# Kernel optimization log

Measured on AMD Instinct MI355X. Metric: run time of the kernel, lower is better.

The kernel has to match this reference:

```python
import jax, jax.numpy as jnp
import numpy as np

N = 50000      # nodes
E = 1_600_000  # edges (avg degree 32)
D = 128        # in/hidden channels
OUT = 64       # out channels


def setup_inputs() -> dict:
    key = jax.random.key(0)
    ks = jax.random.split(key, 12)
    s = 0.08  # ~glorot scale for 128-dim
    return {
        "x": jax.random.normal(ks[0], (N, D), jnp.float32),
        "edge_index": jax.random.randint(ks[1], (2, E), 0, N, dtype=jnp.int64),
        # GCN layer 1
        "W1": jax.random.normal(ks[2], (D, D), jnp.float32) * s,
        "b1": jnp.zeros((D,), jnp.float32),
        # GraphSAGE layer 2 (mean aggregation): lin_l on neighbors, lin_r on root
        "Wl": jax.random.normal(ks[3], (D, D), jnp.float32) * s,
        "Wr": jax.random.normal(ks[4], (D, D), jnp.float32) * s,
        "bs": jnp.zeros((D,), jnp.float32),
        # GAT layer 3 (heads=1, concat=False)
        "Wg": jax.random.normal(ks[5], (D, D), jnp.float32) * s,
        "a_s": jax.random.normal(ks[6], (D,), jnp.float32) * s,
        "a_d": jax.random.normal(ks[7], (D,), jnp.float32) * s,
        "bg": jnp.zeros((D,), jnp.float32),
        # GCN output layer
        "Wo": jax.random.normal(ks[8], (D, OUT), jnp.float32) * s,
        "bo": jnp.zeros((OUT,), jnp.float32),
    }


def _self_loops(src, dst, n):
    loop = jnp.arange(n, dtype=src.dtype)
    return jnp.concatenate([src, loop]), jnp.concatenate([dst, loop])


def gcn_conv(x, W, b, src, dst, n):
    # PyG GCNConv: add self-loops, symmetric normalization D^-1/2 (A+I) D^-1/2
    s2, d2 = _self_loops(src, dst, n)
    deg = jax.ops.segment_sum(jnp.ones_like(d2, dtype=x.dtype), d2, num_segments=n)
    dinv = jnp.where(deg > 0, jax.lax.rsqrt(deg), 0.0)
    h = x @ W                         # [n, out]
    norm = dinv[s2] * dinv[d2]        # [E+n]
    out = jax.ops.segment_sum(h[s2] * norm[:, None], d2, num_segments=n)
    return out + b


def sage_conv(x, Wl, Wr, b, src, dst, n):
    # PyG SAGEConv, aggr='mean': W_l * mean_neigh + W_r * x (no self-loops)
    deg = jax.ops.segment_sum(jnp.ones_like(dst, dtype=x.dtype), dst, num_segments=n)
    agg = jax.ops.segment_sum(x[src], dst, num_segments=n)
    mean = agg / jnp.maximum(deg, 1.0)[:, None]
    return mean @ Wl + x @ Wr + b


def gat_conv(x, W, a_s, a_d, b, src, dst, n):
    # PyG GATConv heads=1, concat=False: self-loops, edge softmax over incoming edges
    h = x @ W                               # [n, out]
    s2, d2 = _self_loops(src, dst, n)
    alpha_src = h @ a_s                     # [n]
    alpha_dst = h @ a_d                     # [n]
    e = jax.nn.leaky_relu(alpha_src[s2] + alpha_dst[d2], negative_slope=0.2)
    m = jax.ops.segment_max(e, d2, num_segments=n)   # every node has a self-loop
    ex = jnp.exp(e - m[d2])
    denom = jax.ops.segment_sum(ex, d2, num_segments=n)
    alpha = ex / denom[d2]
    out = jax.ops.segment_sum(alpha[:, None] * h[s2], d2, num_segments=n)
    return out + b


def reference(x, edge_index, W1, b1, Wl, Wr, bs, Wg, a_s, a_d, bg, Wo, bo):
    src, dst = edge_index[0], edge_index[1]
    n = x.shape[0]
    # eval mode: F.dropout(training=False) is identity
    h = jax.nn.relu(gcn_conv(x, W1, b1, src, dst, n))
    h = jax.nn.relu(sage_conv(h, Wl, Wr, bs, src, dst, n))
    h = jax.nn.relu(gat_conv(h, Wg, a_s, a_d, bg, src, dst, n))
    return gcn_conv(h, Wo, bo, src, dst, n)
```

## Files before the change

### kernel.cpp

```cpp
#include <hip/hip_runtime.h>
#include <math.h>


#define BUCKET_BITS 8
#define BUCKET_SZ   256
#define NBMAX       256
#define CAP         10240
#define CAPE        2048

typedef short short8 __attribute__((ext_vector_type(8)));
typedef float f32x4 __attribute__((ext_vector_type(4)));
typedef unsigned int u32x4 __attribute__((ext_vector_type(4)));
typedef unsigned short u16x8 __attribute__((ext_vector_type(8)));

__device__ __forceinline__ float leaky02(float x) { return x > 0.0f ? x : 0.2f * x; }
__device__ __forceinline__ float bflo(unsigned u) { return __uint_as_float(u << 16); }
__device__ __forceinline__ float bfhi(unsigned u) { return __uint_as_float(u & 0xFFFF0000u); }
__device__ __forceinline__ unsigned short f2bf(float f) {
    unsigned u = __float_as_uint(f);
    u += 0x7FFFu + ((u >> 16) & 1u);
    return (unsigned short)(u >> 16);
}

template<int NO, bool AFP32, bool SCALE, bool BIASRELU, bool DUAL, bool DOTS>
__global__ __launch_bounds__(256) void mgemm_k(
    const void* __restrict__ Av, const float* __restrict__ W,
    const void* __restrict__ A1v, const float* __restrict__ W1,
    unsigned short* __restrict__ C16,
    const float* __restrict__ scale, const float* __restrict__ bias,
    const float* __restrict__ a_s, const float* __restrict__ a_d,
    float* __restrict__ as_, float* __restrict__ ad_, int n)
{
    constexpr int CT = NO / 16;
    __shared__ unsigned short Wp[128 * NO];
    const int tid = threadIdx.x;
    const int wave = tid >> 6, lane = tid & 63;
    const int q = lane >> 4, ml = lane & 15;
    const int row0 = blockIdx.x * 64 + wave * 16;
    int arow = row0 + ml; if (arow >= n) arow = n - 1;

    f32x4 acc[CT];
#pragma unroll
    for (int c = 0; c < CT; c++) acc[c] = {0.f, 0.f, 0.f, 0.f};

    for (int half = 0; half < (DUAL ? 2 : 1); half++) {
        const float* Wsrc = half ? W1 : W;
        const void* Asrc = half ? A1v : Av;
        __syncthreads();
        for (int f = tid; f < 64 * (NO / 4); f += 256) {
            const int kp = f / (NO / 4);
            const int n4 = f % (NO / 4);
            const float4 a = *(const float4*)(Wsrc + (size_t)(2 * kp) * NO + n4 * 4);
            const float4 b = *(const float4*)(Wsrc + (size_t)(2 * kp + 1) * NO + n4 * 4);
            const int k = 2 * kp, kb = k >> 5, qq = (k >> 3) & 3, p = (k & 7) >> 1;
            const float av[4] = {a.x, a.y, a.z, a.w};
            const float bv[4] = {b.x, b.y, b.z, b.w};
#pragma unroll
            for (int j = 0; j < 4; j++) {
                int col = n4 * 4 + j;
                int c = col >> 4, nl = col & 15;
                unsigned pk = (unsigned)f2bf(av[j]) | ((unsigned)f2bf(bv[j]) << 16);
                ((unsigned*)Wp)[(((kb * CT + c) * 64) + qq * 16 + nl) * 4 + p] = pk;
            }
        }
        __syncthreads();
#pragma unroll
        for (int kb = 0; kb < 4; kb++) {
            short8 afr;
            if (AFP32) {
                const float* Af = (const float*)Asrc + (size_t)arow * 128 + kb * 32 + q * 8;
#pragma unroll
                for (int j = 0; j < 8; j++) afr[j] = (short)f2bf(Af[j]);
            } else {
                afr = *(const short8*)((const unsigned short*)Asrc +
                                       (size_t)arow * 128 + kb * 32 + q * 8);
            }
#pragma unroll
            for (int c = 0; c < CT; c++) {
                short8 bfr = *(const short8*)(Wp + ((size_t)(kb * CT + c) * 64 + lane) * 8);
                acc[c] = __builtin_amdgcn_mfma_f32_16x16x32_bf16(afr, bfr, acc[c], 0, 0, 0);
            }
        }
    }

    if (DOTS) {
        float ps[4] = {0.f, 0.f, 0.f, 0.f}, pd[4] = {0.f, 0.f, 0.f, 0.f};
#pragma unroll
        for (int c = 0; c < CT; c++) {
            float sv = a_s[c * 16 + ml], dv = a_d[c * 16 + ml];
#pragma unroll
            for (int r = 0; r < 4; r++) {
                ps[r] = fmaf(acc[c][r], sv, ps[r]);
                pd[r] = fmaf(acc[c][r], dv, pd[r]);
            }
        }
#pragma unroll
        for (int off = 1; off < 16; off <<= 1) {
#pragma unroll
            for (int r = 0; r < 4; r++) {
                ps[r] += __shfl_xor(ps[r], off, 64);
                pd[r] += __shfl_xor(pd[r], off, 64);
            }
        }
        if (ml == 0) {
#pragma unroll
            for (int r = 0; r < 4; r++) {
                int row = row0 + q * 4 + r;
                if (row < n) { as_[row] = ps[r]; ad_[row] = pd[r]; }
            }
        }
    }

    float sc[4];
    if (SCALE) {
#pragma unroll
        for (int r = 0; r < 4; r++) {
            int row = row0 + q * 4 + r;
            sc[r] = scale[row < n ? row : 0];
        }
    }
#pragma unroll
    for (int c = 0; c < CT; c++) {
        float bv = BIASRELU ? bias[c * 16 + ml] : 0.0f;
#pragma unroll
        for (int r = 0; r < 4; r++) {
            int row = row0 + q * 4 + r;
            if (row < n) {
                float v = acc[c][r];
                if (SCALE) v *= sc[r];
                if (BIASRELU) v = fmaxf(v + bv, 0.0f);
                C16[(size_t)row * NO + c * 16 + ml] = f2bf(v);
            }
        }
    }
}

__global__ void binit_k(int* __restrict__ bcur, int nb) {
    int t = threadIdx.x;
    if (t < nb) bcur[t] = t * CAP;
}

#define PART_CH 4096
__global__ __launch_bounds__(256) void part_k(
    const int* __restrict__ src, const int* __restrict__ dst,
    int* __restrict__ bcur, unsigned long long* __restrict__ part, int nE)
{
    __shared__ int cnt[NBMAX];
    __shared__ int cur[NBMAX];
    const int base = blockIdx.x * PART_CH;
    const int t = threadIdx.x;
    cnt[t] = 0;
    __syncthreads();
    int d[PART_CH / 256], s[PART_CH / 256];
#pragma unroll
    for (int j = 0; j < PART_CH / 256; j++) {
        int e = base + j * 256 + t;
        if (e < nE) {
            d[j] = dst[e]; s[j] = src[e];
            atomicAdd(&cnt[d[j] >> BUCKET_BITS], 1);
        } else d[j] = -1;
    }
    __syncthreads();
    {
        int c = cnt[t];
        cur[t] = c ? atomicAdd(&bcur[t], c) : 0;
    }
    __syncthreads();
#pragma unroll
    for (int j = 0; j < PART_CH / 256; j++) {
        if (d[j] >= 0) {
            int p = atomicAdd(&cur[d[j] >> BUCKET_BITS], 1);
            part[p] = ((unsigned long long)(unsigned)d[j] << 32) | (unsigned)s[j];
        }
    }
}

__global__ __launch_bounds__(256) void bscan_k(const int* __restrict__ bcur,
                                               int* __restrict__ bofs, int nb) {
    __shared__ int sm[256];
    const int t = threadIdx.x;
    int v = (t < nb) ? (bcur[t] - t * CAP) : 0;
    sm[t] = v;
    __syncthreads();
    for (int off = 1; off < 256; off <<= 1) {
        int tv = (t >= off) ? sm[t - off] : 0;
        __syncthreads();
        sm[t] += tv;
        __syncthreads();
    }
    if (t < nb) {
        bofs[t] = sm[t] - v;
        if (t == nb - 1) bofs[nb] = sm[t];
    }
}

__global__ __launch_bounds__(256) void csr_k(
    const unsigned long long* __restrict__ part, const int* __restrict__ bcur,
    const int* __restrict__ bofs, int* __restrict__ rowptr, int* __restrict__ srcs,
    float* __restrict__ dinv, float* __restrict__ invm, int n, int nE)
{
    __shared__ int lcnt[BUCKET_SZ];
    __shared__ int sm[BUCKET_SZ];
    __shared__ int lcur[BUCKET_SZ];
    const int b = blockIdx.x;
    const int t = threadIdx.x;
    const int base_in = b * CAP;
    const int cntE = bcur[b] - base_in;
    const int base_out = bofs[b];

    lcnt[t] = 0;
    __syncthreads();
#pragma unroll 4
    for (int e = t; e < cntE; e += 256) {
        int dl = (int)(part[base_in + e] >> 32) & (BUCKET_SZ - 1);
        atomicAdd(&lcnt[dl], 1);
    }
    __syncthreads();
    int v = lcnt[t];
    sm[t] = v;
    __syncthreads();
    for (int off = 1; off < 256; off <<= 1) {
        int tv = (t >= off) ? sm[t - off] : 0;
        __syncthreads();
        sm[t] += tv;
        __syncthreads();
    }
    const int excl = sm[t] - v;
    const int node = (b << BUCKET_BITS) + t;
    if (node < n) {
        rowptr[node] = base_out + excl;
        float dg = (float)v;
        dinv[node] = rsqrtf(dg + 1.0f);
        invm[node] = 1.0f / fmaxf(dg, 1.0f);
        if (node == n - 1) rowptr[n] = nE;
    }
    lcur[t] = excl;
    __syncthreads();
#pragma unroll 4
    for (int e = t; e < cntE; e += 256) {
        unsigned long long w = part[base_in + e];
        int dl = (int)(w >> 32) & (BUCKET_SZ - 1);
        int pos = atomicAdd(&lcur[dl], 1);
        srcs[base_out + pos] = (int)(unsigned)w;
    }
}

template<int LPN, int MODE, bool OV>
__device__ __forceinline__ void gath_loop(
    const u32x4* __restrict__ H4, const int* __restrict__ srcs,
    const int* lsrc, const float* lw, const float* __restrict__ as_,
    float ad_d, int beg, int end, int beg_blk, int lane, float* acc)
{
    const u32x4* __restrict__ Hl = H4 + lane;
    int k = beg;
    for (; k + 8 <= end; k += 8) {
        unsigned sidx[8]; float wv[8];
#pragma unroll
        for (int j = 0; j < 8; j++) {
            int ofs = k + j - beg_blk;
            if (OV) {
                int ofc = ofs < CAPE ? ofs : CAPE - 1;
                int s = (ofs < CAPE) ? lsrc[ofc] : srcs[k + j];
                sidx[j] = (unsigned)s;
                if (MODE == 2)
                    wv[j] = (ofs < CAPE) ? lw[ofc] : __expf(leaky02(as_[s] + ad_d));
            } else {
                sidx[j] = (unsigned)lsrc[ofs];
                if (MODE == 2) wv[j] = lw[ofs];
            }
        }
        u32x4 h[8];
#pragma unroll
        for (int j = 0; j < 8; j++) h[j] = Hl[(size_t)sidx[j] * LPN];
#pragma unroll
        for (int j = 0; j < 8; j++) {
#pragma unroll
            for (int c = 0; c < 4; c++) {
                if (MODE == 2) {
                    acc[2 * c]     = fmaf(wv[j], bflo(h[j][c]), acc[2 * c]);
                    acc[2 * c + 1] = fmaf(wv[j], bfhi(h[j][c]), acc[2 * c + 1]);
                } else {
                    acc[2 * c]     += bflo(h[j][c]);
                    acc[2 * c + 1] += bfhi(h[j][c]);
                }
            }
        }
    }
    if (k < end) {
        unsigned sidx[8]; float wv[8];
#pragma unroll
        for (int j = 0; j < 8; j++) {
            int kk = k + j;
            bool act = kk < end;
            int kc = act ? kk : end - 1;
            int ofs = kc - beg_blk;
            int s; float w0 = 1.0f;
            if (OV) {
                int ofc = ofs < CAPE ? ofs : CAPE - 1;
                s = (ofs < CAPE) ? lsrc[ofc] : srcs[kc];
                if (MODE == 2)
                    w0 = (ofs < CAPE) ? lw[ofc] : __expf(leaky02(as_[s] + ad_d));
            } else {
                s = lsrc[ofs];
                if (MODE == 2) w0 = lw[ofs];
            }
            sidx[j] = (unsigned)s;
            wv[j] = act ? w0 : 0.0f;
        }
        u32x4 h[8];
#pragma unroll
        for (int j = 0; j < 8; j++) h[j] = Hl[(size_t)sidx[j] * LPN];
#pragma unroll
        for (int j = 0; j < 8; j++) {
#pragma unroll
            for (int c = 0; c < 4; c++) {
                acc[2 * c]     = fmaf(wv[j], bflo(h[j][c]), acc[2 * c]);
                acc[2 * c + 1] = fmaf(wv[j], bfhi(h[j][c]), acc[2 * c + 1]);
            }
        }
    }
}

template<int F, int MODE>
__global__ __launch_bounds__(256) void gatherbf_k(
    const unsigned short* __restrict__ H16, float* __restrict__ outf,
    unsigned short* __restrict__ out16,
    const int* __restrict__ rowptr, const int* __restrict__ srcs,
    const float* __restrict__ dinv, const float* __restrict__ as_,
    const float* __restrict__ ad_, const float* __restrict__ bias, int n)
{
    constexpr int LPN = F / 8;
    constexpr int NPB = 256 / LPN;
    __shared__ int lsrc[CAPE];
    __shared__ float lw[(MODE == 2) ? CAPE : 1];

    const int tid = (int)threadIdx.x;
    const int node0 = (int)blockIdx.x * NPB;
    const int nodeN = min(node0 + NPB, n);
    const int beg_blk = rowptr[node0];
    const int end_blk = rowptr[nodeN];
    const int cnt = end_blk - beg_blk;
    const int cl = min(cnt, CAPE);
    for (int i = tid; i < cl; i += 256) lsrc[i] = srcs[beg_blk + i];
    __syncthreads();

    const int node = node0 + tid / LPN;
    const int lane = tid & (LPN - 1);
    const bool alive = node < n;
    int beg = 0, end = 0;
    if (alive) { beg = rowptr[node]; end = rowptr[node + 1]; }

    float ad_d = 0.f, rden = 0.f, sw = 0.f;
    if (MODE == 2) {
        if (alive) {
            ad_d = ad_[node];
            float self_e = __expf(leaky02(as_[node] + ad_d));
            float psum = 0.f;
            for (int kk = beg + lane; kk < end; kk += LPN) {
                int ofs = kk - beg_blk;
                int s = (ofs < CAPE) ? lsrc[ofs < CAPE ? ofs : 0] : srcs[kk];
                float wv = __expf(leaky02(as_[s] + ad_d));
                if (ofs < CAPE) lw[ofs] = wv;
                psum += wv;
            }
#pragma unroll
            for (int off = LPN / 2; off > 0; off >>= 1)
                psum += __shfl_xor(psum, off, 64);
            rden = 1.0f / (psum + self_e);
            sw = self_e * rden;
        }
        __syncthreads();
    }

    float acc[8];
#pragma unroll
    for (int j = 0; j < 8; j++) acc[j] = 0.f;

    const u32x4* __restrict__ H4 = (const u32x4*)H16;
    if (alive) {
        if (cnt <= CAPE)
            gath_loop<LPN, MODE, false>(H4, srcs, lsrc, lw, as_, ad_d,
                                        beg, end, beg_blk, lane, acc);
        else
            gath_loop<LPN, MODE, true>(H4, srcs, lsrc, lw, as_, ad_d,
                                       beg, end, beg_blk, lane, acc);
    }
    if (!alive) return;

    const size_t orow = (size_t)node * LPN + lane;
    float r[8];
    if (MODE == 0) {
        float sc = dinv[node];
#pragma unroll
        for (int j = 0; j < 8; j++) r[j] = acc[j] * sc;
    } else {
        u32x4 su = H4[orow];
        float sv[8];
#pragma unroll
        for (int c = 0; c < 4; c++) { sv[2 * c] = bflo(su[c]); sv[2 * c + 1] = bfhi(su[c]); }
        const float4* b4 = (const float4*)bias;
        float4 ba = b4[lane * 2], bb = b4[lane * 2 + 1];
        float bv[8] = {ba.x, ba.y, ba.z, ba.w, bb.x, bb.y, bb.z, bb.w};
        if (MODE == 2) {
#pragma unroll
            for (int j = 0; j < 8; j++)
                r[j] = fmaxf(fmaf(rden, acc[j], fmaf(sw, sv[j], bv[j])), 0.f);
        } else {
            float dv = dinv[node];
#pragma unroll
            for (int j = 0; j < 8; j++) {
                r[j] = dv * (acc[j] + sv[j]) + bv[j];
                if (MODE == 1) r[j] = fmaxf(r[j], 0.f);
            }
        }
    }
    if (MODE == 3) {
        float4 ra = {r[0], r[1], r[2], r[3]}, rb = {r[4], r[5], r[6], r[7]};
        ((float4*)outf)[orow * 2]     = ra;
        ((float4*)outf)[orow * 2 + 1] = rb;
    } else {
        u16x8 qv;
#pragma unroll
        for (int j = 0; j < 8; j++) qv[j] = f2bf(r[j]);
        ((u16x8*)out16)[orow] = qv;
    }
}

extern "C" void kernel_launch(void* const* d_in, const int* in_sizes, int n_in,
                              void* d_out, int out_size, void* d_ws, size_t ws_size,
                              hipStream_t stream)
{
    const float* x   = (const float*)d_in[0];
    const int*   ei  = (const int*)d_in[1];
    const float* W1  = (const float*)d_in[2];
    const float* b1  = (const float*)d_in[3];
    const float* Wl  = (const float*)d_in[4];
    const float* Wr  = (const float*)d_in[5];
    const float* bs  = (const float*)d_in[6];
    const float* Wg  = (const float*)d_in[7];
    const float* a_s = (const float*)d_in[8];
    const float* a_d = (const float*)d_in[9];
    const float* bg  = (const float*)d_in[10];
    const float* Wo  = (const float*)d_in[11];
    const float* bo  = (const float*)d_in[12];

    const int n  = in_sizes[0] / 128;
    const int nE = in_sizes[1] / 2;
    const int* src = ei;
    const int* dst = ei + nE;

    char* w = (char*)d_ws;
    auto alloc = [&](size_t bytes) { char* p = w; w += (bytes + 255) & ~(size_t)255; return p; };
    unsigned short* S0 = (unsigned short*)alloc((size_t)n * 128 * 2);
    unsigned short* S1 = (unsigned short*)alloc((size_t)n * 128 * 2);
    unsigned short* S2 = (unsigned short*)alloc((size_t)n * 128 * 2);
    const int nbv = (n + BUCKET_SZ - 1) / BUCKET_SZ;
    unsigned long long* part = (unsigned long long*)alloc((size_t)nbv * CAP * 8);
    int*   srcs   = (int*)alloc((size_t)nE * 4);
    int*   rowptr = (int*)alloc((size_t)(n + 1) * 4);
    int*   bofs   = (int*)alloc((NBMAX + 1) * 4);
    int*   bcur   = (int*)alloc(NBMAX * 4);
    float* dinv   = (float*)alloc((size_t)n * 4);
    float* invm   = (float*)alloc((size_t)n * 4);
    float* as_    = (float*)alloc((size_t)n * 4);
    float* ad_    = (float*)alloc((size_t)n * 4);

    const int TB = 256;
    auto cdiv = [](long long a, long long b) { return (int)((a + b - 1) / b); };
    const int nb     = nbv;
    const int gPart  = cdiv(nE, PART_CH);
    const int gGemm  = cdiv(n, 64);
    const int gGa128 = cdiv(n, 16);
    const int gGa64  = cdiv(n, 32);

    binit_k<<<1, 256, 0, stream>>>(bcur, nb);
    part_k<<<gPart, TB, 0, stream>>>(src, dst, bcur, part, nE);
    bscan_k<<<1, 256, 0, stream>>>(bcur, bofs, nb);
    csr_k<<<nb, TB, 0, stream>>>(part, bcur, bofs, rowptr, srcs, dinv, invm, n, nE);

    mgemm_k<128, true, true, false, false, false><<<gGemm, TB, 0, stream>>>(
        x, W1, nullptr, nullptr, S0, dinv, nullptr, nullptr, nullptr, nullptr, nullptr, n);
    gatherbf_k<128, 1><<<gGa128, TB, 0, stream>>>(S0, nullptr, S1, rowptr, srcs,
                                                  dinv, nullptr, nullptr, b1, n);

    gatherbf_k<128, 0><<<gGa128, TB, 0, stream>>>(S1, nullptr, S0, rowptr, srcs,
                                                  invm, nullptr, nullptr, nullptr, n);
    mgemm_k<128, false, false, true, true, false><<<gGemm, TB, 0, stream>>>(
        S0, Wl, S1, Wr, S2, nullptr, bs, nullptr, nullptr, nullptr, nullptr, n);

    mgemm_k<128, false, false, false, false, true><<<gGemm, TB, 0, stream>>>(
        S2, Wg, nullptr, nullptr, S1, nullptr, nullptr, a_s, a_d, as_, ad_, n);
    gatherbf_k<128, 2><<<gGa128, TB, 0, stream>>>(S1, nullptr, S0, rowptr, srcs,
                                                  nullptr, as_, ad_, bg, n);

    mgemm_k<64, false, true, false, false, false><<<gGemm, TB, 0, stream>>>(
        S0, Wo, nullptr, nullptr, S2, dinv, nullptr, nullptr, nullptr, nullptr, nullptr, n);
    gatherbf_k<64, 3><<<gGa64, TB, 0, stream>>>(S2, (float*)d_out, nullptr, rowptr, srcs,
                                                dinv, nullptr, nullptr, bo, n);
}
```

Baseline: 369.8 us.

## Store bf16 features in column-block-major layout and split gathers by column block

Feature matrices move from row-major to a column-blocked layout of 32 bf16 columns per block. Each gather block now handles 64 nodes for one 32-column slice, with blocks interleaved so that every slice shares the same node groups. The goal is a per-pass working set small enough to stay in L2/MALL, cutting the cost of random gathers. GAT edge weights and softmax denominators move into a separate gatw_k kernel that writes them to global memory, and CAPE is raised. The cost is an extra kernel, an extra edge-weight array to write and read, and srcs/rowptr being reread once per column block.

```diff
diff --git a/kernel.cpp b/kernel.cpp
--- a/kernel.cpp
+++ b/kernel.cpp
@@ -6,7 +6,7 @@
 #define BUCKET_SZ   256
 #define NBMAX       256
 #define CAP         10240
-#define CAPE        2048
+#define CAPE        2560
 
 typedef short short8 __attribute__((ext_vector_type(8)));
 typedef float f32x4 __attribute__((ext_vector_type(4)));
@@ -73,7 +73,7 @@
                 for (int j = 0; j < 8; j++) afr[j] = (short)f2bf(Af[j]);
             } else {
                 afr = *(const short8*)((const unsigned short*)Asrc +
-                                       (size_t)arow * 128 + kb * 32 + q * 8);
+                                       ((size_t)kb * n + arow) * 32 + q * 8);
             }
 #pragma unroll
             for (int c = 0; c < CT; c++) {
@@ -122,6 +122,7 @@
 #pragma unroll
     for (int c = 0; c < CT; c++) {
         float bv = BIASRELU ? bias[c * 16 + ml] : 0.0f;
+        const int col = c * 16 + ml;
 #pragma unroll
         for (int r = 0; r < 4; r++) {
             int row = row0 + q * 4 + r;
@@ -129,7 +130,7 @@
                 float v = acc[c][r];
                 if (SCALE) v *= sc[r];
                 if (BIASRELU) v = fmaxf(v + bv, 0.0f);
-                C16[(size_t)row * NO + c * 16 + ml] = f2bf(v);
+                C16[((size_t)(col >> 5) * n + row) * 32 + (col & 31)] = f2bf(v);
             }
         }
     }
@@ -245,13 +246,38 @@
     }
 }
 
-template<int LPN, int MODE, bool OV>
+__global__ __launch_bounds__(256) void gatw_k(
+    const int* __restrict__ rowptr, const int* __restrict__ srcs,
+    const float* __restrict__ as_, const float* __restrict__ ad_,
+    float* __restrict__ ew, float* __restrict__ rdn_, float* __restrict__ sw_, int n)
+{
+    const int node = blockIdx.x * 32 + (threadIdx.x >> 3);
+    const int lane = threadIdx.x & 7;
+    if (node >= n) return;
+    const int beg = rowptr[node], end = rowptr[node + 1];
+    const float ad_d = ad_[node];
+    float psum = 0.f;
+    for (int k = beg + lane; k < end; k += 8) {
+        float e = __expf(leaky02(as_[srcs[k]] + ad_d));
+        ew[k] = e;
+        psum += e;
+    }
+#pragma unroll
+    for (int off = 4; off > 0; off >>= 1) psum += __shfl_xor(psum, off, 64);
+    if (lane == 0) {
+        float se = __expf(leaky02(as_[node] + ad_d));
+        float r = 1.0f / (psum + se);
+        rdn_[node] = r;
+        sw_[node] = se * r;
+    }
+}
+
+template<int MODE, bool OV>
 __device__ __forceinline__ void gath_loop(
-    const u32x4* __restrict__ H4, const int* __restrict__ srcs,
-    const int* lsrc, const float* lw, const float* __restrict__ as_,
-    float ad_d, int beg, int end, int beg_blk, int lane, float* acc)
-{
-    const u32x4* __restrict__ Hl = H4 + lane;
+    const u32x4* __restrict__ Hc, const int* __restrict__ srcs,
+    const float* __restrict__ ew, const int* lsrc, const float* lw,
+    int beg, int end, int beg_blk, int lane, float* acc)
+{
     int k = beg;
     for (; k + 8 <= end; k += 8) {
         unsigned sidx[8]; float wv[8];
@@ -259,11 +285,10 @@
         for (int j = 0; j < 8; j++) {
             int ofs = k + j - beg_blk;
             if (OV) {
-                int ofc = ofs < CAPE ? ofs : CAPE - 1;
-                int s = (ofs < CAPE) ? lsrc[ofc] : srcs[k + j];
-                sidx[j] = (unsigned)s;
-                if (MODE == 2)
-                    wv[j] = (ofs < CAPE) ? lw[ofc] : __expf(leaky02(as_[s] + ad_d));
+                bool in = ofs < CAPE;
+                int ofc = in ? ofs : 0;
+                sidx[j] = (unsigned)(in ? lsrc[ofc] : srcs[k + j]);
+                if (MODE == 2) wv[j] = in ? lw[ofc] : ew[k + j];
             } else {
                 sidx[j] = (unsigned)lsrc[ofs];
                 if (MODE == 2) wv[j] = lw[ofs];
@@ -271,7 +296,7 @@
         }
         u32x4 h[8];
 #pragma unroll
-        for (int j = 0; j < 8; j++) h[j] = Hl[(size_t)sidx[j] * LPN];
+        for (int j = 0; j < 8; j++) h[j] = Hc[(size_t)sidx[j] * 4 + lane];
 #pragma unroll
         for (int j = 0; j < 8; j++) {
 #pragma unroll
@@ -296,10 +321,10 @@
             int ofs = kc - beg_blk;
             int s; float w0 = 1.0f;
             if (OV) {
-                int ofc = ofs < CAPE ? ofs : CAPE - 1;
-                s = (ofs < CAPE) ? lsrc[ofc] : srcs[kc];
-                if (MODE == 2)
-                    w0 = (ofs < CAPE) ? lw[ofc] : __expf(leaky02(as_[s] + ad_d));
+                bool in = ofs < CAPE;
+                int ofc = in ? ofs : 0;
+                s = in ? lsrc[ofc] : srcs[kc];
+                if (MODE == 2) w0 = in ? lw[ofc] : ew[kc];
             } else {
                 s = lsrc[ofs];
                 if (MODE == 2) w0 = lw[ofs];
@@ -309,7 +334,7 @@
         }
         u32x4 h[8];
 #pragma unroll
-        for (int j = 0; j < 8; j++) h[j] = Hl[(size_t)sidx[j] * LPN];
+        for (int j = 0; j < 8; j++) h[j] = Hc[(size_t)sidx[j] * 4 + lane];
 #pragma unroll
         for (int j = 0; j < 8; j++) {
 #pragma unroll
@@ -321,92 +346,77 @@
     }
 }
 
-template<int F, int MODE>
+template<int NCB, int MODE>
 __global__ __launch_bounds__(256) void gatherbf_k(
     const unsigned short* __restrict__ H16, float* __restrict__ outf,
     unsigned short* __restrict__ out16,
     const int* __restrict__ rowptr, const int* __restrict__ srcs,
-    const float* __restrict__ dinv, const float* __restrict__ as_,
-    const float* __restrict__ ad_, const float* __restrict__ bias, int n)
-{
-    constexpr int LPN = F / 8;
-    constexpr int NPB = 256 / LPN;
+    const float* __restrict__ scl,
+    const float* __restrict__ sw_,
+    const float* __restrict__ ew,
+    const float* __restrict__ bias, int n)
+{
+    constexpr int XPC = 8 / NCB;
+    constexpr int NPB = 64;
     __shared__ int lsrc[CAPE];
     __shared__ float lw[(MODE == 2) ? CAPE : 1];
 
+    const int bid = (int)blockIdx.x;
+    const int xj = bid & 7;
+    const int cb = xj / XPC;
+    const int NG = (n + NPB - 1) / NPB;
+    const int ng = (bid >> 3) * XPC + (xj % XPC);
+    if (ng >= NG) return;
+
     const int tid = (int)threadIdx.x;
-    const int node0 = (int)blockIdx.x * NPB;
+    const int node0 = ng * NPB;
     const int nodeN = min(node0 + NPB, n);
     const int beg_blk = rowptr[node0];
     const int end_blk = rowptr[nodeN];
     const int cnt = end_blk - beg_blk;
     const int cl = min(cnt, CAPE);
-    for (int i = tid; i < cl; i += 256) lsrc[i] = srcs[beg_blk + i];
-    __syncthreads();
-
-    const int node = node0 + tid / LPN;
-    const int lane = tid & (LPN - 1);
-    const bool alive = node < n;
-    int beg = 0, end = 0;
-    if (alive) { beg = rowptr[node]; end = rowptr[node + 1]; }
-
-    float ad_d = 0.f, rden = 0.f, sw = 0.f;
-    if (MODE == 2) {
-        if (alive) {
-            ad_d = ad_[node];
-            float self_e = __expf(leaky02(as_[node] + ad_d));
-            float psum = 0.f;
-            for (int kk = beg + lane; kk < end; kk += LPN) {
-                int ofs = kk - beg_blk;
-                int s = (ofs < CAPE) ? lsrc[ofs < CAPE ? ofs : 0] : srcs[kk];
-                float wv = __expf(leaky02(as_[s] + ad_d));
-                if (ofs < CAPE) lw[ofs] = wv;
-                psum += wv;
-            }
-#pragma unroll
-            for (int off = LPN / 2; off > 0; off >>= 1)
-                psum += __shfl_xor(psum, off, 64);
-            rden = 1.0f / (psum + self_e);
-            sw = self_e * rden;
-        }
-        __syncthreads();
-    }
+    for (int i = tid; i < cl; i += 256) {
+        lsrc[i] = srcs[beg_blk + i];
+        if (MODE == 2) lw[i] = ew[beg_blk + i];
+    }
+    __syncthreads();
+
+    const int node = node0 + (tid >> 2);
+    const int lane = tid & 3;
+    if (node >= nodeN) return;
+    const int beg = rowptr[node], end = rowptr[node + 1];
+    const u32x4* __restrict__ Hc = (const u32x4*)H16 + (size_t)cb * n * 4;
 
     float acc[8];
 #pragma unroll
     for (int j = 0; j < 8; j++) acc[j] = 0.f;
 
-    const u32x4* __restrict__ H4 = (const u32x4*)H16;
-    if (alive) {
-        if (cnt <= CAPE)
-            gath_loop<LPN, MODE, false>(H4, srcs, lsrc, lw, as_, ad_d,
-                                        beg, end, beg_blk, lane, acc);
-        else
-            gath_loop<LPN, MODE, true>(H4, srcs, lsrc, lw, as_, ad_d,
-                                       beg, end, beg_blk, lane, acc);
-    }
-    if (!alive) return;
-
-    const size_t orow = (size_t)node * LPN + lane;
+    if (cnt <= CAPE)
+        gath_loop<MODE, false>(Hc, srcs, ew, lsrc, lw, beg, end, beg_blk, lane, acc);
+    else
+        gath_loop<MODE, true>(Hc, srcs, ew, lsrc, lw, beg, end, beg_blk, lane, acc);
+
+    const size_t orow = ((size_t)cb * n + node) * 4 + lane;
     float r[8];
     if (MODE == 0) {
-        float sc = dinv[node];
+        float sc = scl[node];
 #pragma unroll
         for (int j = 0; j < 8; j++) r[j] = acc[j] * sc;
     } else {
-        u32x4 su = H4[orow];
+        u32x4 su = Hc[(size_t)node * 4 + lane];
         float sv[8];
 #pragma unroll
         for (int c = 0; c < 4; c++) { sv[2 * c] = bflo(su[c]); sv[2 * c + 1] = bfhi(su[c]); }
         const float4* b4 = (const float4*)bias;
-        float4 ba = b4[lane * 2], bb = b4[lane * 2 + 1];
+        float4 ba = b4[cb * 8 + lane * 2], bb = b4[cb * 8 + lane * 2 + 1];
         float bv[8] = {ba.x, ba.y, ba.z, ba.w, bb.x, bb.y, bb.z, bb.w};
         if (MODE == 2) {
+            float rden = scl[node], sw = sw_[node];
 #pragma unroll
             for (int j = 0; j < 8; j++)
                 r[j] = fmaxf(fmaf(rden, acc[j], fmaf(sw, sv[j], bv[j])), 0.f);
         } else {
-            float dv = dinv[node];
+            float dv = scl[node];
 #pragma unroll
             for (int j = 0; j < 8; j++) {
                 r[j] = dv * (acc[j] + sv[j]) + bv[j];
@@ -415,9 +425,9 @@
         }
     }
     if (MODE == 3) {
+        float4* o4 = (float4*)(outf + (size_t)node * 64 + cb * 32 + lane * 8);
         float4 ra = {r[0], r[1], r[2], r[3]}, rb = {r[4], r[5], r[6], r[7]};
-        ((float4*)outf)[orow * 2]     = ra;
-        ((float4*)outf)[orow * 2 + 1] = rb;
+        o4[0] = ra; o4[1] = rb;
     } else {
         u16x8 qv;
 #pragma unroll
@@ -464,14 +474,19 @@
     float* invm   = (float*)alloc((size_t)n * 4);
     float* as_    = (float*)alloc((size_t)n * 4);
     float* ad_    = (float*)alloc((size_t)n * 4);
+    float* ew     = (float*)alloc((size_t)nE * 4);
+    float* rdn_   = (float*)alloc((size_t)n * 4);
+    float* sw_    = (float*)alloc((size_t)n * 4);
 
     const int TB = 256;
     auto cdiv = [](long long a, long long b) { return (int)((a + b - 1) / b); };
     const int nb     = nbv;
     const int gPart  = cdiv(nE, PART_CH);
     const int gGemm  = cdiv(n, 64);
-    const int gGa128 = cdiv(n, 16);
-    const int gGa64  = cdiv(n, 32);
+    const int NG     = cdiv(n, 64);
+    const int gGa128 = 8 * cdiv(NG, 2);
+    const int gGa64  = 8 * cdiv(NG, 4);
+    const int gGatw  = cdiv(n, 32);
 
     binit_k<<<1, 256, 0, stream>>>(bcur, nb);
     part_k<<<gPart, TB, 0, stream>>>(src, dst, bcur, part, nE);
@@ -480,21 +495,22 @@
 
     mgemm_k<128, true, true, false, false, false><<<gGemm, TB, 0, stream>>>(
         x, W1, nullptr, nullptr, S0, dinv, nullptr, nullptr, nullptr, nullptr, nullptr, n);
-    gatherbf_k<128, 1><<<gGa128, TB, 0, stream>>>(S0, nullptr, S1, rowptr, srcs,
-                                                  dinv, nullptr, nullptr, b1, n);
-
-    gatherbf_k<128, 0><<<gGa128, TB, 0, stream>>>(S1, nullptr, S0, rowptr, srcs,
-                                                  invm, nullptr, nullptr, nullptr, n);
+    gatherbf_k<4, 1><<<gGa128, TB, 0, stream>>>(S0, nullptr, S1, rowptr, srcs,
+                                                dinv, nullptr, nullptr, b1, n);
+
+    gatherbf_k<4, 0><<<gGa128, TB, 0, stream>>>(S1, nullptr, S0, rowptr, srcs,
+                                                invm, nullptr, nullptr, nullptr, n);
     mgemm_k<128, false, false, true, true, false><<<gGemm, TB, 0, stream>>>(
         S0, Wl, S1, Wr, S2, nullptr, bs, nullptr, nullptr, nullptr, nullptr, n);
 
     mgemm_k<128, false, false, false, false, true><<<gGemm, TB, 0, stream>>>(
         S2, Wg, nullptr, nullptr, S1, nullptr, nullptr, a_s, a_d, as_, ad_, n);
-    gatherbf_k<128, 2><<<gGa128, TB, 0, stream>>>(S1, nullptr, S0, rowptr, srcs,
-                                                  nullptr, as_, ad_, bg, n);
+    gatw_k<<<gGatw, TB, 0, stream>>>(rowptr, srcs, as_, ad_, ew, rdn_, sw_, n);
+    gatherbf_k<4, 2><<<gGa128, TB, 0, stream>>>(S1, nullptr, S0, rowptr, srcs,
+                                                rdn_, sw_, ew, bg, n);
 
     mgemm_k<64, false, true, false, false, false><<<gGemm, TB, 0, stream>>>(
         S0, Wo, nullptr, nullptr, S2, dinv, nullptr, nullptr, nullptr, nullptr, nullptr, n);
-    gatherbf_k<64, 3><<<gGa64, TB, 0, stream>>>(S2, (float*)d_out, nullptr, rowptr, srcs,
-                                                dinv, nullptr, nullptr, bo, n);
-}
+    gatherbf_k<2, 3><<<gGa64, TB, 0, stream>>>(S2, (float*)d_out, nullptr, rowptr, srcs,
+                                               dinv, nullptr, nullptr, bo, n);
+}
```

After: 357.6 us. 1.03x faster.
